# Optimization experiments

Hardware: AMD Instinct MI355X
Metric: run time of the kernel (lower is better)

## Reference

```python
import jax, jax.numpy as jnp
import numpy as np

HIDDEN = 1024
N_HEAD = 16
D_HEAD = HIDDEN // N_HEAD


def setup_inputs() -> dict:
    key = jax.random.key(0)
    ks = jax.random.split(key, 12)
    B, S, H = 2, 2048, HIDDEN
    scale = 1.0 / np.sqrt(H)
    inp = {
        "q": jax.random.normal(ks[0], (B, S, H), jnp.float32),
        "k": jax.random.normal(ks[1], (B, S, H), jnp.float32),
        "v": jax.random.normal(ks[2], (B, S, H), jnp.float32),
        "mask": jnp.ones((B, 1, S, S), jnp.int32),
        "w_q": jax.random.normal(ks[3], (H, H), jnp.float32) * scale,
        "b_q": jnp.zeros((H,), jnp.float32),
        "w_k": jax.random.normal(ks[4], (H, H), jnp.float32) * scale,
        "b_k": jnp.zeros((H,), jnp.float32),
        "w_v": jax.random.normal(ks[5], (H, H), jnp.float32) * scale,
        "b_v": jnp.zeros((H,), jnp.float32),
        "w_o": jax.random.normal(ks[6], (H, H), jnp.float32) * scale,
        "b_o": jnp.zeros((H,), jnp.float32),
    }
    return inp


def reference(q, k, v, mask, w_q, b_q, w_k, b_k, w_v, b_v, w_o, b_o):
    B, Sq, H = q.shape
    Sk = k.shape[1]
    # projections (weights stored as [in, out])
    qh = (q @ w_q + b_q).reshape(B, Sq, N_HEAD, D_HEAD).transpose(0, 2, 1, 3)
    kh = (k @ w_k + b_k).reshape(B, Sk, N_HEAD, D_HEAD).transpose(0, 2, 1, 3)
    vh = (v @ w_v + b_v).reshape(B, Sk, N_HEAD, D_HEAD).transpose(0, 2, 1, 3)
    scores = jnp.einsum("bhqd,bhkd->bhqk", qh, kh) * (D_HEAD ** -0.5)
    scores = jnp.where(mask == 0, jnp.float32(-10000.0), scores)
    attn = jax.nn.softmax(scores, axis=-1)
    out = jnp.einsum("bhqk,bhkd->bhqd", attn, vh)
    out = out.transpose(0, 2, 1, 3).reshape(B, Sq, H)
    return out @ w_o + b_o
```

## Files before the change

### kernel.cpp

```cpp
#include <hip/hip_runtime.h>
#include <hip/hip_bf16.h>
#include <stdint.h>

#define S_LEN 2048
#define HID   1024
#define NHEAD 16
#define DHEAD 64
#define BATCH 2

#define QSCALE 0.18033688f
#define MASKNEG -14427.0f

typedef __bf16 bf16_t;
typedef __bf16 bf16x4 __attribute__((ext_vector_type(4)));
typedef __bf16 bf16x8 __attribute__((ext_vector_type(8)));
typedef float  f32x4  __attribute__((ext_vector_type(4)));

__device__ __forceinline__ void gl_lds16(const bf16_t* g, bf16_t* l) {
  __builtin_amdgcn_global_load_lds((const __attribute__((address_space(1))) void*)g,
                                   (__attribute__((address_space(3))) void*)l,
                                   16, 0, 0);
}

template<int TR, int TC>
__device__ __forceinline__ void stage_tile(const bf16_t* __restrict__ g, int ldg,
                                           bf16_t* lds, int wave, int lane) {
  constexpr int CH = TC / 8;
  constexpr int NINST = (TR * CH) / 64;
  #pragma unroll
  for (int i = wave; i < NINST; i += 4) {
    int slot = i * 64 + lane;
    int r  = slot / CH;
    int cs = slot & (CH - 1);
    int c  = cs ^ (r & (CH - 1));
    gl_lds16(g + (size_t)r * ldg + c * 8, lds + i * 512);
  }
}

template<int TR>
__device__ __forceinline__ void stage_cvt_tile(const float* __restrict__ g, int ldg,
                                               bf16_t* lds, int tid) {
  constexpr int NSLOT = TR * 8;
  #pragma unroll
  for (int i = 0; i < NSLOT / 256; ++i) {
    int slot = i * 256 + tid;
    int r  = slot >> 3;
    int cs = slot & 7;
    int c  = cs ^ (r & 7);
    const float4* src = (const float4*)(g + (size_t)r * ldg + c * 8);
    float4 u0 = src[0], u1 = src[1];
    bf16x8 o = {(bf16_t)u0.x, (bf16_t)u0.y, (bf16_t)u0.z, (bf16_t)u0.w,
                (bf16_t)u1.x, (bf16_t)u1.y, (bf16_t)u1.z, (bf16_t)u1.w};
    *(bf16x8*)(lds + slot * 8) = o;
  }
}

template<int CH>
__device__ __forceinline__ bf16x8 frag_ld(const bf16_t* lds, int row, int kchunk) {
  int cs = kchunk ^ (row & (CH - 1));
  return *(const bf16x8*)(lds + (row * CH + cs) * 8);
}

__global__ __launch_bounds__(256) void transpose_w4(
    const float* __restrict__ w0, const float* __restrict__ w1,
    const float* __restrict__ w2, const float* __restrict__ w3,
    bf16_t* __restrict__ wt) {
  __shared__ float t[64][65];
  const float* W = blockIdx.z == 0 ? w0 : blockIdx.z == 1 ? w1 : blockIdx.z == 2 ? w2 : w3;
  bf16_t* WT = wt + (size_t)blockIdx.z * HID * HID;
  int tx = threadIdx.x & 63, ty = threadIdx.x >> 6;
  int r0 = blockIdx.y * 64, c0 = blockIdx.x * 64;
  #pragma unroll
  for (int i = ty; i < 64; i += 4) t[i][tx] = W[(size_t)(r0 + i) * HID + c0 + tx];
  __syncthreads();
  #pragma unroll
  for (int i = ty; i < 64; i += 4) WT[(size_t)(c0 + i) * HID + r0 + tx] = (bf16_t)t[tx][i];
}

__global__ __launch_bounds__(256) void mask_flags(const int* __restrict__ mask,
                                                  unsigned char* __restrict__ flags) {
  int qtile = blockIdx.x, b = blockIdx.y;
  const int* base = mask + (size_t)b * S_LEN * S_LEN + (size_t)(qtile * 128) * S_LEN;
  int tid = threadIdx.x;
  int kt = tid >> 4;
  int ok = 1;
  for (int r = 0; r < 128; ++r) {
    const int4* p = (const int4*)(base + (size_t)r * S_LEN + tid * 8);
    int4 a = p[0], c = p[1];
    ok &= (a.x != 0) & (a.y != 0) & (a.z != 0) & (a.w != 0) &
          (c.x != 0) & (c.y != 0) & (c.z != 0) & (c.w != 0);
  }
  __shared__ int oks[16];
  if (tid < 16) oks[tid] = 1;
  __syncthreads();
  if (!ok) atomicAnd(&oks[kt], 0);
  __syncthreads();
  if (tid < 16) flags[(b * 16 + qtile) * 16 + tid] = (unsigned char)oks[tid];
}

__global__ __launch_bounds__(256) void qkv_gemm(
    const float* __restrict__ qf, const float* __restrict__ kf32, const float* __restrict__ vf32,
    const bf16_t* __restrict__ wT,
    const float* __restrict__ bq, const float* __restrict__ bk, const float* __restrict__ bv,
    bf16_t* __restrict__ Qh, bf16_t* __restrict__ Kh, bf16_t* __restrict__ VhT) {
  int mode = blockIdx.z;
  const float*  A    = mode == 0 ? qf : mode == 1 ? kf32 : vf32;
  const bf16_t* Bt   = wT + (size_t)mode * HID * HID;
  const float*  bias = mode == 0 ? bq : mode == 1 ? bk : bv;

  __shared__ __align__(16) bf16_t As[128 * 64];
  __shared__ __align__(16) bf16_t Bs[128 * 64];

  int tid = threadIdx.x, wave = tid >> 6, lane = tid & 63;
  int lane15 = lane & 15, quad = lane >> 4;
  int m0 = blockIdx.x * 128, n0 = blockIdx.y * 128;
  int wm = (wave >> 1) * 64, wn = (wave & 1) * 64;

  f32x4 zero4 = {0.f, 0.f, 0.f, 0.f};
  f32x4 acc[4][4];
  #pragma unroll
  for (int t = 0; t < 4; ++t)
    #pragma unroll
    for (int n = 0; n < 4; ++n) acc[t][n] = zero4;

  for (int k0 = 0; k0 < HID; k0 += 64) {
    stage_cvt_tile<128>(A + (size_t)m0 * HID + k0, HID, As, tid);
    stage_tile<128, 64>(Bt + (size_t)n0 * HID + k0, HID, Bs, wave, lane);
    __syncthreads();
    #pragma unroll
    for (int kc = 0; kc < 2; ++kc) {
      bf16x8 af[4], bfr[4];
      #pragma unroll
      for (int t = 0; t < 4; ++t) af[t]  = frag_ld<8>(As, wm + t * 16 + lane15, kc * 4 + quad);
      #pragma unroll
      for (int n = 0; n < 4; ++n) bfr[n] = frag_ld<8>(Bs, wn + n * 16 + lane15, kc * 4 + quad);
      if (mode < 2) {
        #pragma unroll
        for (int t = 0; t < 4; ++t)
          #pragma unroll
          for (int n = 0; n < 4; ++n)
            acc[t][n] = __builtin_amdgcn_mfma_f32_16x16x32_bf16(af[t], bfr[n], acc[t][n], 0, 0, 0);
      } else {
        #pragma unroll
        for (int t = 0; t < 4; ++t)
          #pragma unroll
          for (int n = 0; n < 4; ++n)
            acc[t][n] = __builtin_amdgcn_mfma_f32_16x16x32_bf16(bfr[n], af[t], acc[t][n], 0, 0, 0);
      }
    }
    __syncthreads();
  }

  if (mode < 2) {
    float sc = (mode == 0) ? QSCALE : 1.0f;
    bf16_t* dst = (mode == 0 ? Qh : Kh);
    #pragma unroll
    for (int t = 0; t < 4; ++t) {
      #pragma unroll
      for (int n = 0; n < 4; ++n) {
        int col = n0 + wn + n * 16 + lane15;
        float bb = bias[col];
        #pragma unroll
        for (int i = 0; i < 4; ++i) {
          int row = m0 + wm + t * 16 + quad * 4 + i;
          bf16_t o = (bf16_t)((acc[t][n][i] + bb) * sc);
          int b = row >> 11, s = row & 2047;
          int h = col >> 6,  d = col & 63;
          dst[((size_t)(b * NHEAD + h) * S_LEN + s) * DHEAD + d] = o;
        }
      }
    }
  } else {
    #pragma unroll
    for (int n = 0; n < 4; ++n) {
      int dbase = n0 + wn + n * 16 + quad * 4;
      float4 bb4 = *(const float4*)(bias + dbase);
      #pragma unroll
      for (int t = 0; t < 4; ++t) {
        int token = m0 + wm + t * 16 + lane15;
        int b = token >> 11, s = token & 2047;
        #pragma unroll
        for (int i = 0; i < 4; ++i) {
          int dg = dbase + i;
          int h = dg >> 6, d = dg & 63;
          float bb = i == 0 ? bb4.x : i == 1 ? bb4.y : i == 2 ? bb4.z : bb4.w;
          VhT[((size_t)(b * NHEAD + h) * DHEAD + d) * S_LEN + s] = (bf16_t)(acc[t][n][i] + bb);
        }
      }
    }
  }
}

__global__ __launch_bounds__(256) void attn_kernel(
    const bf16_t* __restrict__ Qh, const bf16_t* __restrict__ Kh, const bf16_t* __restrict__ VhT,
    const int* __restrict__ mask, const unsigned char* __restrict__ flags,
    bf16_t* __restrict__ O) {
  __shared__ __align__(16) bf16_t Ks[128 * 64];
  __shared__ __align__(16) bf16_t VTs[80 * 128];
  __shared__ __align__(16) bf16_t Ps[128 * 128];

  int tid = threadIdx.x, wave = tid >> 6, lane = tid & 63;
  int lane15 = lane & 15, quad = lane >> 4;
  int bh = blockIdx.y, b = bh >> 4, h = bh & 15;
  int qt = blockIdx.x;
  int wrow = wave * 32;

  if (tid < 128) VTs[64 * 128 + tid] = (bf16_t)1.0f;

  stage_tile<128, 64>(Qh + ((size_t)bh * S_LEN + qt * 128) * DHEAD, DHEAD, Ps, wave, lane);
  __syncthreads();
  bf16x8 qa[2][2];
  #pragma unroll
  for (int kc = 0; kc < 2; ++kc)
    #pragma unroll
    for (int nq = 0; nq < 2; ++nq)
      qa[kc][nq] = frag_ld<8>(Ps, wrow + nq * 16 + lane15, kc * 4 + quad);

  f32x4 zero4 = {0.f, 0.f, 0.f, 0.f};
  f32x4 o_acc[2][5];
  #pragma unroll
  for (int nq = 0; nq < 2; ++nq)
    #pragma unroll
    for (int mt = 0; mt < 5; ++mt) o_acc[nq][mt] = zero4;

  for (int kt = 0; kt < S_LEN / 128; ++kt) {
    stage_tile<128, 64>(Kh + ((size_t)bh * S_LEN + kt * 128) * DHEAD, DHEAD, Ks, wave, lane);
    stage_tile<64, 128>(VhT + (size_t)bh * DHEAD * S_LEN + kt * 128, S_LEN, VTs, wave, lane);
    __syncthreads();

    f32x4 sa[2][8];
    #pragma unroll
    for (int nq = 0; nq < 2; ++nq)
      #pragma unroll
      for (int mc = 0; mc < 8; ++mc) sa[nq][mc] = zero4;
    #pragma unroll
    for (int kc = 0; kc < 2; ++kc) {
      bf16x8 kf[8];
      #pragma unroll
      for (int mc = 0; mc < 8; ++mc) kf[mc] = frag_ld<8>(Ks, mc * 16 + lane15, kc * 4 + quad);
      #pragma unroll
      for (int nq = 0; nq < 2; ++nq)
        #pragma unroll
        for (int mc = 0; mc < 8; ++mc)
          sa[nq][mc] = __builtin_amdgcn_mfma_f32_16x16x32_bf16(kf[mc], qa[kc][nq], sa[nq][mc], 0, 0, 0);
    }

    if (flags[(b * 16 + qt) * 16 + kt] == 0) {
      #pragma unroll
      for (int nq = 0; nq < 2; ++nq)
        #pragma unroll
        for (int mc = 0; mc < 8; ++mc)
          #pragma unroll
          for (int i = 0; i < 4; ++i) {
            int q = qt * 128 + wrow + nq * 16 + lane15;
            int c = kt * 128 + mc * 16 + quad * 4 + i;
            if (mask[(size_t)b * S_LEN * S_LEN + (size_t)q * S_LEN + c] == 0)
              sa[nq][mc][i] = MASKNEG;
          }
    }

    #pragma unroll
    for (int nq = 0; nq < 2; ++nq) {
      int q = wrow + nq * 16 + lane15;
      #pragma unroll
      for (int mc = 0; mc < 8; ++mc) {
        bf16x4 pk = {(bf16_t)exp2f(sa[nq][mc][0]), (bf16_t)exp2f(sa[nq][mc][1]),
                     (bf16_t)exp2f(sa[nq][mc][2]), (bf16_t)exp2f(sa[nq][mc][3])};
        int chunk = mc * 2 + (quad >> 1);
        int slot = chunk ^ (q & 15);
        *(bf16x4*)(Ps + q * 128 + slot * 8 + (quad & 1) * 4) = pk;
      }
    }

    #pragma unroll
    for (int kc = 0; kc < 4; ++kc) {
      bf16x8 vf[5], pf[2];
      #pragma unroll
      for (int mt = 0; mt < 5; ++mt) vf[mt] = frag_ld<16>(VTs, mt * 16 + lane15, kc * 4 + quad);
      #pragma unroll
      for (int nq = 0; nq < 2; ++nq) pf[nq] = frag_ld<16>(Ps, wrow + nq * 16 + lane15, kc * 4 + quad);
      #pragma unroll
      for (int nq = 0; nq < 2; ++nq)
        #pragma unroll
        for (int mt = 0; mt < 5; ++mt)
          o_acc[nq][mt] = __builtin_amdgcn_mfma_f32_16x16x32_bf16(vf[mt], pf[nq], o_acc[nq][mt], 0, 0, 0);
    }
    __syncthreads();
  }

  #pragma unroll
  for (int nq = 0; nq < 2; ++nq) {
    float lval = __shfl(o_acc[nq][4][0], lane15);
    float inv = 1.0f / lval;
    int s = qt * 128 + wrow + nq * 16 + lane15;
    size_t orow = ((size_t)b * S_LEN + s) * HID + h * DHEAD;
    #pragma unroll
    for (int mt = 0; mt < 4; ++mt) {
      bf16x4 ov = {(bf16_t)(o_acc[nq][mt][0] * inv), (bf16_t)(o_acc[nq][mt][1] * inv),
                   (bf16_t)(o_acc[nq][mt][2] * inv), (bf16_t)(o_acc[nq][mt][3] * inv)};
      *(bf16x4*)(O + orow + mt * 16 + quad * 4) = ov;
    }
  }
}

__global__ __launch_bounds__(256) void oproj_gemm(
    const bf16_t* __restrict__ A, const bf16_t* __restrict__ Bt,
    const float* __restrict__ bias, float* __restrict__ out) {
  __shared__ __align__(16) bf16_t As[128 * 64];
  __shared__ __align__(16) bf16_t Bs[128 * 64];

  int tid = threadIdx.x, wave = tid >> 6, lane = tid & 63;
  int lane15 = lane & 15, quad = lane >> 4;
  int m0 = blockIdx.x * 128, n0 = blockIdx.y * 128;
  int wm = (wave >> 1) * 64, wn = (wave & 1) * 64;

  f32x4 zero4 = {0.f, 0.f, 0.f, 0.f};
  f32x4 acc[4][4];
  #pragma unroll
  for (int t = 0; t < 4; ++t)
    #pragma unroll
    for (int n = 0; n < 4; ++n) acc[t][n] = zero4;

  for (int k0 = 0; k0 < HID; k0 += 64) {
    stage_tile<128, 64>(A  + (size_t)m0 * HID + k0, HID, As, wave, lane);
    stage_tile<128, 64>(Bt + (size_t)n0 * HID + k0, HID, Bs, wave, lane);
    __syncthreads();
    #pragma unroll
    for (int kc = 0; kc < 2; ++kc) {
      bf16x8 af[4], bfr[4];
      #pragma unroll
      for (int t = 0; t < 4; ++t) af[t]  = frag_ld<8>(As, wm + t * 16 + lane15, kc * 4 + quad);
      #pragma unroll
      for (int n = 0; n < 4; ++n) bfr[n] = frag_ld<8>(Bs, wn + n * 16 + lane15, kc * 4 + quad);
      #pragma unroll
      for (int t = 0; t < 4; ++t)
        #pragma unroll
        for (int n = 0; n < 4; ++n)
          acc[t][n] = __builtin_amdgcn_mfma_f32_16x16x32_bf16(af[t], bfr[n], acc[t][n], 0, 0, 0);
    }
    __syncthreads();
  }

  #pragma unroll
  for (int t = 0; t < 4; ++t) {
    #pragma unroll
    for (int n = 0; n < 4; ++n) {
      int col = n0 + wn + n * 16 + lane15;
      float bb = bias[col];
      #pragma unroll
      for (int i = 0; i < 4; ++i) {
        int row = m0 + wm + t * 16 + quad * 4 + i;
        out[(size_t)row * HID + col] = acc[t][n][i] + bb;
      }
    }
  }
}

extern "C" void kernel_launch(void* const* d_in, const int* in_sizes, int n_in,
                              void* d_out, int out_size, void* d_ws, size_t ws_size,
                              hipStream_t stream) {
  (void)in_sizes; (void)n_in; (void)out_size; (void)ws_size;
  const float* q  = (const float*)d_in[0];
  const float* k  = (const float*)d_in[1];
  const float* v  = (const float*)d_in[2];
  const int*  mask = (const int*)d_in[3];
  const float* wq = (const float*)d_in[4];
  const float* bq = (const float*)d_in[5];
  const float* wk = (const float*)d_in[6];
  const float* bk = (const float*)d_in[7];
  const float* wv = (const float*)d_in[8];
  const float* bv = (const float*)d_in[9];
  const float* wo = (const float*)d_in[10];
  const float* bo = (const float*)d_in[11];

  char* ws = (char*)d_ws;
  bf16_t* wT    = (bf16_t*)(ws);
  bf16_t* Qh    = (bf16_t*)(ws + (8u  << 20));
  bf16_t* Kh    = (bf16_t*)(ws + (16u << 20));
  bf16_t* VhT   = (bf16_t*)(ws + (24u << 20));
  bf16_t* Obuf  = (bf16_t*)(ws + (32u << 20));
  unsigned char* flags = (unsigned char*)(ws + (40u << 20));

  transpose_w4<<<dim3(16, 16, 4), 256, 0, stream>>>(wq, wk, wv, wo, wT);
  mask_flags<<<dim3(16, 2), 256, 0, stream>>>(mask, flags);
  qkv_gemm<<<dim3(32, 8, 3), 256, 0, stream>>>(q, k, v, wT, bq, bk, bv, Qh, Kh, VhT);
  attn_kernel<<<dim3(16, 32), 256, 0, stream>>>(Qh, Kh, VhT, mask, flags, Obuf);
  oproj_gemm<<<dim3(32, 8), 256, 0, stream>>>(Obuf, wT + (size_t)3 * HID * HID, bo, (float*)d_out);
}
```

Before: 315.5 us.

## Parallelize mask scan and prefetch fp32 A tiles in registers in QKV GEMM

The mask-flag kernel now runs 8x more blocks, each scanning 16 rows, and combines results through global atomicAnd on int flags. Those flags are initialised to all-ones by the first block of the weight-transpose kernel. In the QKV GEMM, the next fp32 A tile is loaded into registers while MFMAs run on the current tile, removing the trailing barrier, and occupancy is hinted with waves_per_eu(3). The aim is to fix the under-parallelised mask scan (only 32 blocks before) and hide global load latency in the GEMM. The cost is higher register pressure and a dependence on kernel ordering for the flag initialisation.

New measurement: 489.1 us. +55.0%, slower.

```diff
diff --git a/kernel.cpp b/kernel.cpp
--- a/kernel.cpp
+++ b/kernel.cpp
@@ -37,24 +37,6 @@
   }
 }
 
-template<int TR>
-__device__ __forceinline__ void stage_cvt_tile(const float* __restrict__ g, int ldg,
-                                               bf16_t* lds, int tid) {
-  constexpr int NSLOT = TR * 8;
-  #pragma unroll
-  for (int i = 0; i < NSLOT / 256; ++i) {
-    int slot = i * 256 + tid;
-    int r  = slot >> 3;
-    int cs = slot & 7;
-    int c  = cs ^ (r & 7);
-    const float4* src = (const float4*)(g + (size_t)r * ldg + c * 8);
-    float4 u0 = src[0], u1 = src[1];
-    bf16x8 o = {(bf16_t)u0.x, (bf16_t)u0.y, (bf16_t)u0.z, (bf16_t)u0.w,
-                (bf16_t)u1.x, (bf16_t)u1.y, (bf16_t)u1.z, (bf16_t)u1.w};
-    *(bf16x8*)(lds + slot * 8) = o;
-  }
-}
-
 template<int CH>
 __device__ __forceinline__ bf16x8 frag_ld(const bf16_t* lds, int row, int kchunk) {
   int cs = kchunk ^ (row & (CH - 1));
@@ -64,7 +46,11 @@
 __global__ __launch_bounds__(256) void transpose_w4(
     const float* __restrict__ w0, const float* __restrict__ w1,
     const float* __restrict__ w2, const float* __restrict__ w3,
-    bf16_t* __restrict__ wt) {
+    bf16_t* __restrict__ wt, int* __restrict__ flags) {
+  if (blockIdx.x == 0 && blockIdx.y == 0 && blockIdx.z == 0) {
+    flags[threadIdx.x] = -1;
+    flags[threadIdx.x + 256] = -1;
+  }
   __shared__ float t[64][65];
   const float* W = blockIdx.z == 0 ? w0 : blockIdx.z == 1 ? w1 : blockIdx.z == 2 ? w2 : w3;
   bf16_t* WT = wt + (size_t)blockIdx.z * HID * HID;
@@ -78,27 +64,30 @@
 }
 
 __global__ __launch_bounds__(256) void mask_flags(const int* __restrict__ mask,
-                                                  unsigned char* __restrict__ flags) {
-  int qtile = blockIdx.x, b = blockIdx.y;
-  const int* base = mask + (size_t)b * S_LEN * S_LEN + (size_t)(qtile * 128) * S_LEN;
+                                                  int* __restrict__ flags) {
+  int qtile = blockIdx.x, rg = blockIdx.y, b = blockIdx.z;
+  const int* base = mask + (size_t)b * S_LEN * S_LEN
+                  + (size_t)(qtile * 128 + rg * 16) * S_LEN;
   int tid = threadIdx.x;
   int kt = tid >> 4;
   int ok = 1;
-  for (int r = 0; r < 128; ++r) {
+  #pragma unroll
+  for (int r = 0; r < 16; ++r) {
     const int4* p = (const int4*)(base + (size_t)r * S_LEN + tid * 8);
     int4 a = p[0], c = p[1];
     ok &= (a.x != 0) & (a.y != 0) & (a.z != 0) & (a.w != 0) &
           (c.x != 0) & (c.y != 0) & (c.z != 0) & (c.w != 0);
   }
   __shared__ int oks[16];
-  if (tid < 16) oks[tid] = 1;
+  if (tid < 16) oks[tid] = -1;
   __syncthreads();
   if (!ok) atomicAnd(&oks[kt], 0);
   __syncthreads();
-  if (tid < 16) flags[(b * 16 + qtile) * 16 + tid] = (unsigned char)oks[tid];
-}
-
-__global__ __launch_bounds__(256) void qkv_gemm(
+  if (tid < 16 && oks[tid] == 0) atomicAnd(&flags[(b * 16 + qtile) * 16 + tid], 0);
+}
+
+__global__ __launch_bounds__(256) __attribute__((amdgpu_waves_per_eu(3)))
+void qkv_gemm(
     const float* __restrict__ qf, const float* __restrict__ kf32, const float* __restrict__ vf32,
     const bf16_t* __restrict__ wT,
     const float* __restrict__ bq, const float* __restrict__ bk, const float* __restrict__ bv,
@@ -123,10 +112,42 @@
     #pragma unroll
     for (int n = 0; n < 4; ++n) acc[t][n] = zero4;
 
-  for (int k0 = 0; k0 < HID; k0 += 64) {
-    stage_cvt_tile<128>(A + (size_t)m0 * HID + k0, HID, As, tid);
+  const float* Abase = A + (size_t)m0 * HID;
+  int soff[4];
+  #pragma unroll
+  for (int i = 0; i < 4; ++i) {
+    int slot = i * 256 + tid;
+    int r = slot >> 3;
+    int c = (slot & 7) ^ (r & 7);
+    soff[i] = r * HID + c * 8;
+  }
+
+  float4 apre[4][2];
+  #pragma unroll
+  for (int i = 0; i < 4; ++i) {
+    const float4* src = (const float4*)(Abase + soff[i]);
+    apre[i][0] = src[0]; apre[i][1] = src[1];
+  }
+
+  for (int it = 0; it < 16; ++it) {
+    int k0 = it * 64;
+    __syncthreads();
+    #pragma unroll
+    for (int i = 0; i < 4; ++i) {
+      float4 u0 = apre[i][0], u1 = apre[i][1];
+      bf16x8 o = {(bf16_t)u0.x, (bf16_t)u0.y, (bf16_t)u0.z, (bf16_t)u0.w,
+                  (bf16_t)u1.x, (bf16_t)u1.y, (bf16_t)u1.z, (bf16_t)u1.w};
+      *(bf16x8*)(As + (i * 256 + tid) * 8) = o;
+    }
     stage_tile<128, 64>(Bt + (size_t)n0 * HID + k0, HID, Bs, wave, lane);
     __syncthreads();
+    if (it < 15) {
+      #pragma unroll
+      for (int i = 0; i < 4; ++i) {
+        const float4* src = (const float4*)(Abase + (k0 + 64) + soff[i]);
+        apre[i][0] = src[0]; apre[i][1] = src[1];
+      }
+    }
     #pragma unroll
     for (int kc = 0; kc < 2; ++kc) {
       bf16x8 af[4], bfr[4];
@@ -148,7 +169,6 @@
             acc[t][n] = __builtin_amdgcn_mfma_f32_16x16x32_bf16(bfr[n], af[t], acc[t][n], 0, 0, 0);
       }
     }
-    __syncthreads();
   }
 
   if (mode < 2) {
@@ -193,7 +213,7 @@
 
 __global__ __launch_bounds__(256) void attn_kernel(
     const bf16_t* __restrict__ Qh, const bf16_t* __restrict__ Kh, const bf16_t* __restrict__ VhT,
-    const int* __restrict__ mask, const unsigned char* __restrict__ flags,
+    const int* __restrict__ mask, const int* __restrict__ flags,
     bf16_t* __restrict__ O) {
   __shared__ __align__(16) bf16_t Ks[128 * 64];
   __shared__ __align__(16) bf16_t VTs[80 * 128];
@@ -379,10 +399,10 @@
   bf16_t* Kh    = (bf16_t*)(ws + (16u << 20));
   bf16_t* VhT   = (bf16_t*)(ws + (24u << 20));
   bf16_t* Obuf  = (bf16_t*)(ws + (32u << 20));
-  unsigned char* flags = (unsigned char*)(ws + (40u << 20));
-
-  transpose_w4<<<dim3(16, 16, 4), 256, 0, stream>>>(wq, wk, wv, wo, wT);
-  mask_flags<<<dim3(16, 2), 256, 0, stream>>>(mask, flags);
+  int* flags    = (int*)(ws + (40u << 20));
+
+  transpose_w4<<<dim3(16, 16, 4), 256, 0, stream>>>(wq, wk, wv, wo, wT, flags);
+  mask_flags<<<dim3(16, 8, 2), 256, 0, stream>>>(mask, flags);
   qkv_gemm<<<dim3(32, 8, 3), 256, 0, stream>>>(q, k, v, wT, bq, bk, bv, Qh, Kh, VhT);
   attn_kernel<<<dim3(16, 32), 256, 0, stream>>>(Qh, Kh, VhT, mask, flags, Obuf);
   oproj_gemm<<<dim3(32, 8), 256, 0, stream>>>(Obuf, wT + (size_t)3 * HID * HID, bo, (float*)d_out);
```
